# Kernel tuning notes

Hardware: AMD Instinct MI355X
Metric: run time of the kernel (lower is better)

## Reference

```python
import jax, jax.numpy as jnp
import numpy as np

D = 768       # input_size
C = 8000      # num_classes
S = 4096      # seq_len
B = 2         # batch
SCALE = 1.0
LN_EPS = 1e-5


def setup_inputs() -> dict:
    key = jax.random.key(0)
    ks = jax.random.split(key, 8)
    std = 0.03  # module's _init_weights std
    return {
        "x": jax.random.normal(ks[0], (B, S, D), dtype=jnp.float32),
        "encoded_descriptions": jax.random.normal(ks[1], (C, D), dtype=jnp.float32),
        "Wk": jax.random.normal(ks[2], (D, D), dtype=jnp.float32) * std,
        "Wv": jax.random.normal(ks[3], (D, D), dtype=jnp.float32) * std,
        "bv": jax.random.normal(ks[4], (D,), dtype=jnp.float32) * 0.01,
        "ln_gamma": jnp.ones((D,), dtype=jnp.float32),
        "ln_beta": jnp.zeros((D,), dtype=jnp.float32),
        "out_w": jax.random.normal(ks[5], (D,), dtype=jnp.float32) * std,
        "out_b": jax.random.normal(ks[6], (), dtype=jnp.float32) * 0.01,
    }


def reference(x, encoded_descriptions, Wk, Wv, bv, ln_gamma, ln_beta, out_w, out_b):
    # V = x @ Wv^T + bv ; K = x @ Wk^T  (torch Linear applies weight transposed)
    V = jnp.einsum('bsd,ed->bse', x, Wv) + bv          # [B, S, D]
    K = jnp.einsum('bsd,ed->bse', x, Wk)               # [B, S, D]
    # att_weights = Q @ K^T, Q broadcast over batch -> [B, C, S]
    att = jnp.einsum('cd,bsd->bcs', encoded_descriptions, K)
    attention = jax.nn.softmax(att / SCALE, axis=2)    # [B, C, S]
    y = jnp.einsum('bcs,bsd->bcd', attention, V)       # [B, C, D]
    # LayerNorm over last dim
    mu = jnp.mean(y, axis=-1, keepdims=True)
    var = jnp.mean(jnp.square(y - mu), axis=-1, keepdims=True)
    y = (y - mu) * jax.lax.rsqrt(var + LN_EPS) * ln_gamma + ln_beta
    # output = sum over D of out_w * y + out_b  -> [B, C]
    out = jnp.einsum('bcd,d->bc', y, out_w) + out_b
    return out
```

## Files before the change

kernel.cpp:

```cpp
#include <hip/hip_runtime.h>


typedef _Float16 half8  __attribute__((ext_vector_type(8)));
typedef _Float16 half4v __attribute__((ext_vector_type(4)));
typedef float    f32x4  __attribute__((ext_vector_type(4)));
typedef float    f32x16 __attribute__((ext_vector_type(16)));

#define L2E 1.44269504088896340736f

__device__ __forceinline__ void gld_lds16(_Float16* lds, const _Float16* g) {
  __builtin_amdgcn_global_load_lds(
      (const __attribute__((address_space(1))) unsigned int*)g,
      (__attribute__((address_space(3))) unsigned int*)lds, 16, 0, 0);
}

__global__ void cvt_kernel(const float* __restrict__ src, _Float16* __restrict__ dst, int n4) {
  int i = blockIdx.x * blockDim.x + threadIdx.x;
  if (i >= n4) return;
  float4 v = reinterpret_cast<const float4*>(src)[i];
  half4v h; h[0] = (_Float16)v.x; h[1] = (_Float16)v.y; h[2] = (_Float16)v.z; h[3] = (_Float16)v.w;
  reinterpret_cast<half4v*>(dst)[i] = h;
}

template <int MODE>
__global__ __launch_bounds__(256, 2) void gemm_nt_f16(
    const _Float16* __restrict__ A, const _Float16* __restrict__ Bt,
    _Float16* __restrict__ C, const float* __restrict__ bias, int M, int N)
{
  __shared__ __align__(16) _Float16 As[2][128 * 64];
  __shared__ __align__(16) _Float16 Bs[2][128 * 64];
  const int tid = threadIdx.x;
  const int lane = tid & 63, wid = tid >> 6;
  const int ntn = N >> 7;
  const int mtile = blockIdx.x / ntn, ntile = blockIdx.x - mtile * ntn;
  const int m0 = mtile << 7, n0 = ntile << 7;
  const int wm = wid >> 1, wn = wid & 1;

  f32x4 acc[4][4] = {};

  auto stage = [&](int buf, int kt) {
#pragma unroll
    for (int j = 0; j < 4; ++j) {
      int idx = (j << 8) + tid;
      int row = idx >> 3, slot = idx & 7;
      int gc = (kt << 6) + ((slot ^ (row & 7)) << 3);
      _Float16* ldsbase_a = &As[buf][(size_t)(((j << 8) + (wid << 6)) << 3)];
      _Float16* ldsbase_b = &Bs[buf][(size_t)(((j << 8) + (wid << 6)) << 3)];
      gld_lds16(ldsbase_a, &A[(size_t)(m0 + row) * 768 + gc]);
      gld_lds16(ldsbase_b, &Bt[(size_t)(n0 + row) * 768 + gc]);
    }
  };

  stage(0, 0);
  __syncthreads();

  for (int kt = 0; kt < 12; ++kt) {
    int cur = kt & 1;
    if (kt < 11) stage(cur ^ 1, kt + 1);
#pragma unroll
    for (int ks = 0; ks < 2; ++ks) {
      half8 a[4], b[4];
      int dloc = (ks << 5) + ((lane >> 4) << 3);
#pragma unroll
      for (int mi = 0; mi < 4; ++mi) {
        int row = (wm << 6) + (mi << 4) + (lane & 15);
        a[mi] = *reinterpret_cast<const half8*>(&As[cur][row * 64 + (dloc ^ ((row & 7) << 3))]);
      }
#pragma unroll
      for (int ni = 0; ni < 4; ++ni) {
        int row = (wn << 6) + (ni << 4) + (lane & 15);
        b[ni] = *reinterpret_cast<const half8*>(&Bs[cur][row * 64 + (dloc ^ ((row & 7) << 3))]);
      }
#pragma unroll
      for (int mi = 0; mi < 4; ++mi)
#pragma unroll
        for (int ni = 0; ni < 4; ++ni)
          acc[mi][ni] = __builtin_amdgcn_mfma_f32_16x16x32_f16(a[mi], b[ni], acc[mi][ni], 0, 0, 0);
    }
    __syncthreads();
  }

#pragma unroll
  for (int mi = 0; mi < 4; ++mi)
#pragma unroll
    for (int ni = 0; ni < 4; ++ni) {
      int col = n0 + (wn << 6) + (ni << 4) + (lane & 15);
#pragma unroll
      for (int r = 0; r < 4; ++r) {
        int row = m0 + (wm << 6) + (mi << 4) + ((lane >> 4) << 2) + r;
        float v = acc[mi][ni][r];
        if (bias) v += bias[row];
        size_t a;
        if (MODE == 1) {
          a = ((size_t)(row >> 5) * 48 + (col >> 4)) * 512 + (row & 31) * 16 + (col & 15);
        } else {
          a = (((size_t)(col >> 12) * 24 + (row >> 5)) * 256 + ((col & 4095) >> 4)) * 512
              + (row & 31) * 16 + (col & 15);
        }
        C[a] = (_Float16)v;
      }
    }
}

#define QS_STRIDE 776
#define PS_STRIDE 264

__global__ __launch_bounds__(512, 4) void attn_kernel(
    const float* __restrict__ Qf, const _Float16* __restrict__ Kf,
    const _Float16* __restrict__ Vf,
    const float* __restrict__ gamma, const float* __restrict__ beta,
    const float* __restrict__ outw, const float* __restrict__ outb,
    float* __restrict__ out)
{
  __shared__ __align__(16) _Float16 Qs[32 * QS_STRIDE];
  __shared__ __align__(16) _Float16 Ps[32 * PS_STRIDE];
  __shared__ float redmax[8 * 32];
  __shared__ float redsum[8 * 32];
  __shared__ float mrow[32], lrow[32], rrow[32];
  __shared__ float gws[768];
  __shared__ float epi[32 * 25];
  __shared__ float scal[2];

  const int tid = threadIdx.x;
  const int lane = tid & 63;
  const int wid = tid >> 6;
  const int l31 = lane & 31;
  const int lh = lane >> 5;

  int xcd = blockIdx.x & 7, i8 = blockIdx.x >> 3;
  int f = (xcd < 4) ? (xcd * 63 + i8) : (252 + (xcd - 4) * 62 + i8);
  const int bb = f / 250;
  const int ct = f - bb * 250;
  const int c0 = ct << 5;

#pragma unroll
  for (int i = 0; i < 12; ++i) {
    int idx = tid + (i << 9);
    int row = idx / 192, c4 = idx - row * 192;
    float4 v = reinterpret_cast<const float4*>(Qf)[(size_t)(c0 + row) * 192 + c4];
    half4v h; h[0] = (_Float16)v.x; h[1] = (_Float16)v.y; h[2] = (_Float16)v.z; h[3] = (_Float16)v.w;
    *reinterpret_cast<half4v*>(&Qs[row * QS_STRIDE + (c4 << 2)]) = h;
  }
  for (int i = tid; i < 768; i += 512) gws[i] = gamma[i] * outw[i];
  if (tid < 32) { mrow[tid] = -1e30f; lrow[tid] = 0.f; }
  __syncthreads();
  if (tid < 64) {
    float g = 0.f, bw = 0.f;
#pragma unroll
    for (int j = 0; j < 12; ++j) { int d = tid + (j << 6); g += gws[d]; bw += beta[d] * outw[d]; }
#pragma unroll
    for (int m = 32; m; m >>= 1) { g += __shfl_xor(g, m); bw += __shfl_xor(bw, m); }
    if (tid == 0) { scal[0] = g; scal[1] = bw; }
  }

  f32x16 acc0 = {}, acc1 = {}, acc2 = {};
  const int n0w = wid * 96;
  const _Float16* qrow = &Qs[l31 * QS_STRIDE + (lh << 3)];
  const int laneoff = l31 * 16 + lh * 8;
  const _Float16* kfb = Kf + ((size_t)(bb * 128 + wid) * 48) * 512 + laneoff;
  const _Float16* vfb = Vf + ((size_t)(bb * 24 + wid * 3) * 256) * 512 + laneoff;

  for (int st = 0; st < 16; ++st) {
    f32x16 qk = {};
    const _Float16* kb = kfb + (size_t)st * (8 * 48 * 512);
    uint4 kp[4];
#pragma unroll
    for (int j = 0; j < 4; ++j) kp[j] = *reinterpret_cast<const uint4*>(kb + j * 512);
#pragma unroll
    for (int k = 0; k < 48; ++k) {
      half8 kf = __builtin_bit_cast(half8, kp[k & 3]);
      if (k < 44) kp[k & 3] = *reinterpret_cast<const uint4*>(kb + (k + 4) * 512);
      half8 qf = *reinterpret_cast<const half8*>(qrow + (k << 4));
      qk = __builtin_amdgcn_mfma_f32_32x32x16_f16(kf, qf, qk, 0, 0, 0);
    }
    const _Float16* vb = vfb + (size_t)st * (16 * 512);
    uint4 vp[2][3];
    vp[0][0] = *reinterpret_cast<const uint4*>(vb);
    vp[0][1] = *reinterpret_cast<const uint4*>(vb + 131072);
    vp[0][2] = *reinterpret_cast<const uint4*>(vb + 262144);

    float mx = fmaxf(fmaxf(fmaxf(qk[0], qk[1]), fmaxf(qk[2], qk[3])),
                     fmaxf(fmaxf(qk[4], qk[5]), fmaxf(qk[6], qk[7])));
    mx = fmaxf(mx, fmaxf(fmaxf(fmaxf(qk[8], qk[9]), fmaxf(qk[10], qk[11])),
                         fmaxf(fmaxf(qk[12], qk[13]), fmaxf(qk[14], qk[15]))));
    mx = fmaxf(mx, __shfl_xor(mx, 32));
    if (lane < 32) redmax[(wid << 5) + l31] = mx;
    __syncthreads();
    if (tid < 32) {
      float pm = redmax[tid];
#pragma unroll
      for (int w = 1; w < 8; ++w) pm = fmaxf(pm, redmax[(w << 5) + tid]);
      float mo = mrow[tid];
      float mn = fmaxf(mo, pm);
      mrow[tid] = mn;
      rrow[tid] = exp2f((mo - mn) * L2E);
    }
    __syncthreads();
    {
      float m = mrow[l31];
      float sum = 0.f;
      int sb = (wid << 5) + (lh << 2);
#pragma unroll
      for (int q2 = 0; q2 < 4; ++q2) {
        float p0 = exp2f((qk[4 * q2 + 0] - m) * L2E);
        float p1 = exp2f((qk[4 * q2 + 1] - m) * L2E);
        float p2 = exp2f((qk[4 * q2 + 2] - m) * L2E);
        float p3 = exp2f((qk[4 * q2 + 3] - m) * L2E);
        sum += (p0 + p1) + (p2 + p3);
        half4v h; h[0] = (_Float16)p0; h[1] = (_Float16)p1; h[2] = (_Float16)p2; h[3] = (_Float16)p3;
        *reinterpret_cast<half4v*>(&Ps[l31 * PS_STRIDE + sb + (q2 << 3)]) = h;
      }
      sum += __shfl_xor(sum, 32);
      if (lane < 32) redsum[(wid << 5) + l31] = sum;
    }
    __syncthreads();
    if ((tid >> 5) == 2) {
      int c = tid & 31;
      float s = redsum[c];
#pragma unroll
      for (int w = 1; w < 8; ++w) s += redsum[(w << 5) + c];
      lrow[c] = lrow[c] * rrow[c] + s;
    }
#pragma unroll
    for (int r = 0; r < 16; ++r) {
      float rs = rrow[(r & 3) + ((r >> 2) << 3) + (lh << 2)];
      acc0[r] *= rs; acc1[r] *= rs; acc2[r] *= rs;
    }
    vp[1][0] = *reinterpret_cast<const uint4*>(vb + 512);
    vp[1][1] = *reinterpret_cast<const uint4*>(vb + 131072 + 512);
    vp[1][2] = *reinterpret_cast<const uint4*>(vb + 262144 + 512);
#pragma unroll
    for (int ks = 0; ks < 16; ++ks) {
      half8 b0 = __builtin_bit_cast(half8, vp[ks & 1][0]);
      half8 b1 = __builtin_bit_cast(half8, vp[ks & 1][1]);
      half8 b2 = __builtin_bit_cast(half8, vp[ks & 1][2]);
      if (ks < 14) {
        vp[ks & 1][0] = *reinterpret_cast<const uint4*>(vb + (ks + 2) * 512);
        vp[ks & 1][1] = *reinterpret_cast<const uint4*>(vb + 131072 + (ks + 2) * 512);
        vp[ks & 1][2] = *reinterpret_cast<const uint4*>(vb + 262144 + (ks + 2) * 512);
      }
      half8 pa = *reinterpret_cast<const half8*>(&Ps[l31 * PS_STRIDE + (ks << 4) + (lh << 3)]);
      acc0 = __builtin_amdgcn_mfma_f32_32x32x16_f16(pa, b0, acc0, 0, 0, 0);
      acc1 = __builtin_amdgcn_mfma_f32_32x32x16_f16(pa, b1, acc1, 0, 0, 0);
      acc2 = __builtin_amdgcn_mfma_f32_32x32x16_f16(pa, b2, acc2, 0, 0, 0);
    }
  }

  float gw0 = gws[n0w + l31];
  float gw1 = gws[n0w + 32 + l31];
  float gw2 = gws[n0w + 64 + l31];
#pragma unroll
  for (int r = 0; r < 16; ++r) {
    float y0 = acc0[r], y1 = acc1[r], y2 = acc2[r];
    float t1 = y0 + y1 + y2;
    float t2 = y0 * y0 + y1 * y1 + y2 * y2;
    float t3 = y0 * gw0 + y1 * gw1 + y2 * gw2;
#pragma unroll
    for (int m = 1; m <= 16; m <<= 1) {
      t1 += __shfl_xor(t1, m); t2 += __shfl_xor(t2, m); t3 += __shfl_xor(t3, m);
    }
    if (l31 == 0) {
      int c = (r & 3) + ((r >> 2) << 3) + (lh << 2);
      float* e = &epi[c * 25 + wid * 3];
      e[0] = t1; e[1] = t2; e[2] = t3;
    }
  }
  __syncthreads();
  if (tid < 32) {
    float S1 = 0.f, S2 = 0.f, S3 = 0.f;
#pragma unroll
    for (int w = 0; w < 8; ++w) {
      const float* e = &epi[tid * 25 + w * 3];
      S1 += e[0]; S2 += e[1]; S3 += e[2];
    }
    float l = lrow[tid];
    float invl = 1.0f / l;
    float mu = S1 * invl * (1.0f / 768.0f);
    float ey2 = S2 * invl * invl * (1.0f / 768.0f);
    float var = ey2 - mu * mu;
    float rs = rsqrtf(var + 1e-5f);
    float res = rs * (S3 * invl - mu * scal[0]) + scal[1] + outb[0];
    out[bb * 8000 + c0 + tid] = res;
  }
}

extern "C" void kernel_launch(void* const* d_in, const int* in_sizes, int n_in,
                              void* d_out, int out_size, void* d_ws, size_t ws_size,
                              hipStream_t stream) {
  (void)in_sizes; (void)n_in; (void)out_size; (void)ws_size;
  const float* x     = (const float*)d_in[0];
  const float* qenc  = (const float*)d_in[1];
  const float* Wk    = (const float*)d_in[2];
  const float* Wv    = (const float*)d_in[3];
  const float* bv    = (const float*)d_in[4];
  const float* gam   = (const float*)d_in[5];
  const float* bet   = (const float*)d_in[6];
  const float* outw  = (const float*)d_in[7];
  const float* outb  = (const float*)d_in[8];
  float* out = (float*)d_out;

  char* ws = (char*)d_ws;
  _Float16* x_h  = (_Float16*)(ws);
  _Float16* wk_h = (_Float16*)(ws + 12582912);
  _Float16* wv_h = (_Float16*)(ws + 13762560);
  _Float16* K_f  = (_Float16*)(ws + 14942208);
  _Float16* V_f  = (_Float16*)(ws + 27525120);

  cvt_kernel<<<6144, 256, 0, stream>>>(x, x_h, 1572864);
  cvt_kernel<<<576, 256, 0, stream>>>(Wk, wk_h, 147456);
  cvt_kernel<<<576, 256, 0, stream>>>(Wv, wv_h, 147456);
  gemm_nt_f16<1><<<384, 256, 0, stream>>>(x_h, wk_h, K_f, nullptr, 8192, 768);
  gemm_nt_f16<2><<<384, 256, 0, stream>>>(wv_h, x_h, V_f, bv, 768, 8192);
  attn_kernel<<<500, 512, 0, stream>>>(qenc, K_f, V_f, gam, bet, outw, outb, out);
}
```

Measured before the change: 347.4 us.

## Process 64 query rows per attention block to reuse K/V loads

Each attention block now handles 64 classes (two 32-row MFMA tiles) instead of 32, so every K and V fragment loaded from global memory feeds twice as many MFMAs. This halves K/V traffic per class and the grid drops to 250 blocks. Softmax running max/sum now live in registers per wave, computed redundantly by every wave, and the rescale factors move across lanes by shuffle, which removes one barrier per step. The cost is double the accumulator registers with launch bounds relaxed to 2 blocks/CU, and only 250 blocks for 256 CUs, so occupancy and latency hiding are lower.

```diff
diff --git a/kernel.cpp b/kernel.cpp
--- a/kernel.cpp
+++ b/kernel.cpp
@@ -105,20 +105,20 @@
 #define QS_STRIDE 776
 #define PS_STRIDE 264
 
-__global__ __launch_bounds__(512, 4) void attn_kernel(
+__global__ __launch_bounds__(512, 2) void attn_kernel(
     const float* __restrict__ Qf, const _Float16* __restrict__ Kf,
     const _Float16* __restrict__ Vf,
     const float* __restrict__ gamma, const float* __restrict__ beta,
     const float* __restrict__ outw, const float* __restrict__ outb,
     float* __restrict__ out)
 {
-  __shared__ __align__(16) _Float16 Qs[32 * QS_STRIDE];
-  __shared__ __align__(16) _Float16 Ps[32 * PS_STRIDE];
-  __shared__ float redmax[8 * 32];
-  __shared__ float redsum[8 * 32];
-  __shared__ float mrow[32], lrow[32], rrow[32];
+  __shared__ __align__(16) _Float16 Qs[64 * QS_STRIDE];
+  __shared__ __align__(16) _Float16 Ps[64 * PS_STRIDE];
+  __shared__ float redmax[8 * 64];
+  __shared__ float redsum[8 * 64];
   __shared__ float gws[768];
-  __shared__ float epi[32 * 25];
+  __shared__ float epi[64 * 25];
+  __shared__ float lrowS[64];
   __shared__ float scal[2];
 
   const int tid = threadIdx.x;
@@ -128,13 +128,13 @@
   const int lh = lane >> 5;
 
   int xcd = blockIdx.x & 7, i8 = blockIdx.x >> 3;
-  int f = (xcd < 4) ? (xcd * 63 + i8) : (252 + (xcd - 4) * 62 + i8);
-  const int bb = f / 250;
-  const int ct = f - bb * 250;
-  const int c0 = ct << 5;
-
-#pragma unroll
-  for (int i = 0; i < 12; ++i) {
+  int f = (xcd < 2) ? (xcd * 32 + i8) : (64 + (xcd - 2) * 31 + i8);
+  const int bb = f / 125;
+  const int ct = f - bb * 125;
+  const int c0 = ct << 6;
+
+#pragma unroll
+  for (int i = 0; i < 24; ++i) {
     int idx = tid + (i << 9);
     int row = idx / 192, c4 = idx - row * 192;
     float4 v = reinterpret_cast<const float4*>(Qf)[(size_t)(c0 + row) * 192 + c4];
@@ -142,7 +142,6 @@
     *reinterpret_cast<half4v*>(&Qs[row * QS_STRIDE + (c4 << 2)]) = h;
   }
   for (int i = tid; i < 768; i += 512) gws[i] = gamma[i] * outw[i];
-  if (tid < 32) { mrow[tid] = -1e30f; lrow[tid] = 0.f; }
   __syncthreads();
   if (tid < 64) {
     float g = 0.f, bw = 0.f;
@@ -153,15 +152,19 @@
     if (tid == 0) { scal[0] = g; scal[1] = bw; }
   }
 
-  f32x16 acc0 = {}, acc1 = {}, acc2 = {};
+  float mrow0 = -1e30f, mrow1 = -1e30f, lrow0 = 0.f, lrow1 = 0.f;
+
+  f32x16 acc00 = {}, acc01 = {}, acc02 = {};
+  f32x16 acc10 = {}, acc11 = {}, acc12 = {};
   const int n0w = wid * 96;
-  const _Float16* qrow = &Qs[l31 * QS_STRIDE + (lh << 3)];
+  const _Float16* qrow0 = &Qs[l31 * QS_STRIDE + (lh << 3)];
+  const _Float16* qrow1 = qrow0 + 32 * QS_STRIDE;
   const int laneoff = l31 * 16 + lh * 8;
   const _Float16* kfb = Kf + ((size_t)(bb * 128 + wid) * 48) * 512 + laneoff;
   const _Float16* vfb = Vf + ((size_t)(bb * 24 + wid * 3) * 256) * 512 + laneoff;
 
   for (int st = 0; st < 16; ++st) {
-    f32x16 qk = {};
+    f32x16 qk0 = {}, qk1 = {};
     const _Float16* kb = kfb + (size_t)st * (8 * 48 * 512);
     uint4 kp[4];
 #pragma unroll
@@ -170,8 +173,10 @@
     for (int k = 0; k < 48; ++k) {
       half8 kf = __builtin_bit_cast(half8, kp[k & 3]);
       if (k < 44) kp[k & 3] = *reinterpret_cast<const uint4*>(kb + (k + 4) * 512);
-      half8 qf = *reinterpret_cast<const half8*>(qrow + (k << 4));
-      qk = __builtin_amdgcn_mfma_f32_32x32x16_f16(kf, qf, qk, 0, 0, 0);
+      half8 qf0 = *reinterpret_cast<const half8*>(qrow0 + (k << 4));
+      half8 qf1 = *reinterpret_cast<const half8*>(qrow1 + (k << 4));
+      qk0 = __builtin_amdgcn_mfma_f32_32x32x16_f16(kf, qf0, qk0, 0, 0, 0);
+      qk1 = __builtin_amdgcn_mfma_f32_32x32x16_f16(kf, qf1, qk1, 0, 0, 0);
     }
     const _Float16* vb = vfb + (size_t)st * (16 * 512);
     uint4 vp[2][3];
@@ -179,56 +184,73 @@
     vp[0][1] = *reinterpret_cast<const uint4*>(vb + 131072);
     vp[0][2] = *reinterpret_cast<const uint4*>(vb + 262144);
 
-    float mx = fmaxf(fmaxf(fmaxf(qk[0], qk[1]), fmaxf(qk[2], qk[3])),
-                     fmaxf(fmaxf(qk[4], qk[5]), fmaxf(qk[6], qk[7])));
-    mx = fmaxf(mx, fmaxf(fmaxf(fmaxf(qk[8], qk[9]), fmaxf(qk[10], qk[11])),
-                         fmaxf(fmaxf(qk[12], qk[13]), fmaxf(qk[14], qk[15]))));
-    mx = fmaxf(mx, __shfl_xor(mx, 32));
-    if (lane < 32) redmax[(wid << 5) + l31] = mx;
+    float mx0 = qk0[0], mx1 = qk1[0];
+#pragma unroll
+    for (int r = 1; r < 16; ++r) { mx0 = fmaxf(mx0, qk0[r]); mx1 = fmaxf(mx1, qk1[r]); }
+    mx0 = fmaxf(mx0, __shfl_xor(mx0, 32));
+    mx1 = fmaxf(mx1, __shfl_xor(mx1, 32));
+    if (lh == 0) {
+      redmax[(wid << 6) + l31] = mx0;
+      redmax[(wid << 6) + 32 + l31] = mx1;
+    }
     __syncthreads();
-    if (tid < 32) {
-      float pm = redmax[tid];
-#pragma unroll
-      for (int w = 1; w < 8; ++w) pm = fmaxf(pm, redmax[(w << 5) + tid]);
-      float mo = mrow[tid];
-      float mn = fmaxf(mo, pm);
-      mrow[tid] = mn;
-      rrow[tid] = exp2f((mo - mn) * L2E);
-    }
-    __syncthreads();
-    {
-      float m = mrow[l31];
-      float sum = 0.f;
-      int sb = (wid << 5) + (lh << 2);
-#pragma unroll
-      for (int q2 = 0; q2 < 4; ++q2) {
-        float p0 = exp2f((qk[4 * q2 + 0] - m) * L2E);
-        float p1 = exp2f((qk[4 * q2 + 1] - m) * L2E);
-        float p2 = exp2f((qk[4 * q2 + 2] - m) * L2E);
-        float p3 = exp2f((qk[4 * q2 + 3] - m) * L2E);
-        sum += (p0 + p1) + (p2 + p3);
-        half4v h; h[0] = (_Float16)p0; h[1] = (_Float16)p1; h[2] = (_Float16)p2; h[3] = (_Float16)p3;
-        *reinterpret_cast<half4v*>(&Ps[l31 * PS_STRIDE + sb + (q2 << 3)]) = h;
-      }
-      sum += __shfl_xor(sum, 32);
-      if (lane < 32) redsum[(wid << 5) + l31] = sum;
-    }
-    __syncthreads();
-    if ((tid >> 5) == 2) {
-      int c = tid & 31;
-      float s = redsum[c];
-#pragma unroll
-      for (int w = 1; w < 8; ++w) s += redsum[(w << 5) + c];
-      lrow[c] = lrow[c] * rrow[c] + s;
+    float pm0 = redmax[l31], pm1 = redmax[32 + l31];
+#pragma unroll
+    for (int w = 1; w < 8; ++w) {
+      pm0 = fmaxf(pm0, redmax[(w << 6) + l31]);
+      pm1 = fmaxf(pm1, redmax[(w << 6) + 32 + l31]);
+    }
+    float mn0 = fmaxf(mrow0, pm0), mn1 = fmaxf(mrow1, pm1);
+    float rr0 = exp2f((mrow0 - mn0) * L2E), rr1 = exp2f((mrow1 - mn1) * L2E);
+    mrow0 = mn0; mrow1 = mn1;
+
+    float sum0 = 0.f, sum1 = 0.f;
+    const int sb = (wid << 5) + (lh << 2);
+#pragma unroll
+    for (int q2 = 0; q2 < 4; ++q2) {
+      float p0 = exp2f((qk0[4 * q2 + 0] - mn0) * L2E);
+      float p1 = exp2f((qk0[4 * q2 + 1] - mn0) * L2E);
+      float p2 = exp2f((qk0[4 * q2 + 2] - mn0) * L2E);
+      float p3 = exp2f((qk0[4 * q2 + 3] - mn0) * L2E);
+      sum0 += (p0 + p1) + (p2 + p3);
+      half4v h; h[0] = (_Float16)p0; h[1] = (_Float16)p1; h[2] = (_Float16)p2; h[3] = (_Float16)p3;
+      *reinterpret_cast<half4v*>(&Ps[l31 * PS_STRIDE + sb + (q2 << 3)]) = h;
+      float u0 = exp2f((qk1[4 * q2 + 0] - mn1) * L2E);
+      float u1 = exp2f((qk1[4 * q2 + 1] - mn1) * L2E);
+      float u2 = exp2f((qk1[4 * q2 + 2] - mn1) * L2E);
+      float u3 = exp2f((qk1[4 * q2 + 3] - mn1) * L2E);
+      sum1 += (u0 + u1) + (u2 + u3);
+      half4v h2; h2[0] = (_Float16)u0; h2[1] = (_Float16)u1; h2[2] = (_Float16)u2; h2[3] = (_Float16)u3;
+      *reinterpret_cast<half4v*>(&Ps[(32 + l31) * PS_STRIDE + sb + (q2 << 3)]) = h2;
+    }
+    sum0 += __shfl_xor(sum0, 32);
+    sum1 += __shfl_xor(sum1, 32);
+    if (lh == 0) {
+      redsum[(wid << 6) + l31] = sum0;
+      redsum[(wid << 6) + 32 + l31] = sum1;
     }
 #pragma unroll
     for (int r = 0; r < 16; ++r) {
-      float rs = rrow[(r & 3) + ((r >> 2) << 3) + (lh << 2)];
-      acc0[r] *= rs; acc1[r] *= rs; acc2[r] *= rs;
+      int crow = (r & 3) + ((r >> 2) << 3) + (lh << 2);
+      float rs0 = __shfl(rr0, crow);
+      float rs1 = __shfl(rr1, crow);
+      acc00[r] *= rs0; acc01[r] *= rs0; acc02[r] *= rs0;
+      acc10[r] *= rs1; acc11[r] *= rs1; acc12[r] *= rs1;
     }
     vp[1][0] = *reinterpret_cast<const uint4*>(vb + 512);
     vp[1][1] = *reinterpret_cast<const uint4*>(vb + 131072 + 512);
     vp[1][2] = *reinterpret_cast<const uint4*>(vb + 262144 + 512);
+    __syncthreads();
+    {
+      float s0 = redsum[l31], s1 = redsum[32 + l31];
+#pragma unroll
+      for (int w = 1; w < 8; ++w) {
+        s0 += redsum[(w << 6) + l31];
+        s1 += redsum[(w << 6) + 32 + l31];
+      }
+      lrow0 = lrow0 * rr0 + s0;
+      lrow1 = lrow1 * rr1 + s1;
+    }
 #pragma unroll
     for (int ks = 0; ks < 16; ++ks) {
       half8 b0 = __builtin_bit_cast(half8, vp[ks & 1][0]);
@@ -239,41 +261,56 @@
         vp[ks & 1][1] = *reinterpret_cast<const uint4*>(vb + 131072 + (ks + 2) * 512);
         vp[ks & 1][2] = *reinterpret_cast<const uint4*>(vb + 262144 + (ks + 2) * 512);
       }
-      half8 pa = *reinterpret_cast<const half8*>(&Ps[l31 * PS_STRIDE + (ks << 4) + (lh << 3)]);
-      acc0 = __builtin_amdgcn_mfma_f32_32x32x16_f16(pa, b0, acc0, 0, 0, 0);
-      acc1 = __builtin_amdgcn_mfma_f32_32x32x16_f16(pa, b1, acc1, 0, 0, 0);
-      acc2 = __builtin_amdgcn_mfma_f32_32x32x16_f16(pa, b2, acc2, 0, 0, 0);
-    }
-  }
-
+      half8 pa0 = *reinterpret_cast<const half8*>(&Ps[l31 * PS_STRIDE + (ks << 4) + (lh << 3)]);
+      half8 pa1 = *reinterpret_cast<const half8*>(&Ps[(32 + l31) * PS_STRIDE + (ks << 4) + (lh << 3)]);
+      acc00 = __builtin_amdgcn_mfma_f32_32x32x16_f16(pa0, b0, acc00, 0, 0, 0);
+      acc01 = __builtin_amdgcn_mfma_f32_32x32x16_f16(pa0, b1, acc01, 0, 0, 0);
+      acc02 = __builtin_amdgcn_mfma_f32_32x32x16_f16(pa0, b2, acc02, 0, 0, 0);
+      acc10 = __builtin_amdgcn_mfma_f32_32x32x16_f16(pa1, b0, acc10, 0, 0, 0);
+      acc11 = __builtin_amdgcn_mfma_f32_32x32x16_f16(pa1, b1, acc11, 0, 0, 0);
+      acc12 = __builtin_amdgcn_mfma_f32_32x32x16_f16(pa1, b2, acc12, 0, 0, 0);
+    }
+  }
+
+  if (wid == 0 && lh == 0) { lrowS[l31] = lrow0; lrowS[32 + l31] = lrow1; }
   float gw0 = gws[n0w + l31];
   float gw1 = gws[n0w + 32 + l31];
   float gw2 = gws[n0w + 64 + l31];
 #pragma unroll
   for (int r = 0; r < 16; ++r) {
-    float y0 = acc0[r], y1 = acc1[r], y2 = acc2[r];
-    float t1 = y0 + y1 + y2;
-    float t2 = y0 * y0 + y1 * y1 + y2 * y2;
-    float t3 = y0 * gw0 + y1 * gw1 + y2 * gw2;
-#pragma unroll
-    for (int m = 1; m <= 16; m <<= 1) {
-      t1 += __shfl_xor(t1, m); t2 += __shfl_xor(t2, m); t3 += __shfl_xor(t3, m);
-    }
-    if (l31 == 0) {
-      int c = (r & 3) + ((r >> 2) << 3) + (lh << 2);
-      float* e = &epi[c * 25 + wid * 3];
-      e[0] = t1; e[1] = t2; e[2] = t3;
+    int c = (r & 3) + ((r >> 2) << 3) + (lh << 2);
+    {
+      float y0 = acc00[r], y1 = acc01[r], y2 = acc02[r];
+      float t1 = y0 + y1 + y2;
+      float t2 = y0 * y0 + y1 * y1 + y2 * y2;
+      float t3 = y0 * gw0 + y1 * gw1 + y2 * gw2;
+#pragma unroll
+      for (int m = 1; m <= 16; m <<= 1) {
+        t1 += __shfl_xor(t1, m); t2 += __shfl_xor(t2, m); t3 += __shfl_xor(t3, m);
+      }
+      if (l31 == 0) { float* e = &epi[c * 25 + wid * 3]; e[0] = t1; e[1] = t2; e[2] = t3; }
+    }
+    {
+      float y0 = acc10[r], y1 = acc11[r], y2 = acc12[r];
+      float t1 = y0 + y1 + y2;
+      float t2 = y0 * y0 + y1 * y1 + y2 * y2;
+      float t3 = y0 * gw0 + y1 * gw1 + y2 * gw2;
+#pragma unroll
+      for (int m = 1; m <= 16; m <<= 1) {
+        t1 += __shfl_xor(t1, m); t2 += __shfl_xor(t2, m); t3 += __shfl_xor(t3, m);
+      }
+      if (l31 == 0) { float* e = &epi[(32 + c) * 25 + wid * 3]; e[0] = t1; e[1] = t2; e[2] = t3; }
     }
   }
   __syncthreads();
-  if (tid < 32) {
+  if (tid < 64) {
     float S1 = 0.f, S2 = 0.f, S3 = 0.f;
 #pragma unroll
     for (int w = 0; w < 8; ++w) {
       const float* e = &epi[tid * 25 + w * 3];
       S1 += e[0]; S2 += e[1]; S3 += e[2];
     }
-    float l = lrow[tid];
+    float l = lrowS[tid];
     float invl = 1.0f / l;
     float mu = S1 * invl * (1.0f / 768.0f);
     float ey2 = S2 * invl * invl * (1.0f / 768.0f);
@@ -311,5 +348,5 @@
   cvt_kernel<<<576, 256, 0, stream>>>(Wv, wv_h, 147456);
   gemm_nt_f16<1><<<384, 256, 0, stream>>>(x_h, wk_h, K_f, nullptr, 8192, 768);
   gemm_nt_f16<2><<<384, 256, 0, stream>>>(wv_h, x_h, V_f, bv, 768, 8192);
-  attn_kernel<<<500, 512, 0, stream>>>(qenc, K_f, V_f, gam, bet, outw, outb, out);
-}
+  attn_kernel<<<250, 512, 0, stream>>>(qenc, K_f, V_f, gam, bet, outw, outb, out);
+}
```

Result: faster. 318.1 us (-8.4%).
